# Optimization experiments

Measured on AMD Instinct MI355X. Metric: run time of the kernel, lower is better.

## Reference

```python
import jax, jax.numpy as jnp
import numpy as np

N = 4_194_304      # number of rays
NUM_ITER = 12      # Newton iterations (fixed)
DAMPING = 0.95
TOL = 1e-6
EPS = 1e-12


def setup_inputs() -> dict:
    key = jax.random.key(0)
    k1, k2 = jax.random.split(key, 2)
    # Rays start on the plane x=-10 inside the aperture, pointing roughly +x.
    yz = jax.random.uniform(k1, (N, 2), minval=-20.0, maxval=20.0)
    P = jnp.concatenate([jnp.full((N, 1), -10.0, jnp.float32), yz], axis=1)
    d = jax.random.normal(k2, (N, 2), dtype=jnp.float32) * 0.05
    V = jnp.concatenate([jnp.ones((N, 1), jnp.float32), d], axis=1)
    V = V / jnp.linalg.norm(V, axis=1, keepdims=True)
    return {
        "P": P,
        "V": V,
        "tf": jnp.eye(4, dtype=jnp.float32),
        "diameter": jnp.float32(50.0),
        "C": jnp.float32(0.02),          # curvature 1/R, R = 50mm
        "anchors": jnp.zeros((2,), jnp.float32),
        "scale": jnp.float32(1.0),
        "normalize": jnp.array(False),
    }


def _translate_x(d):
    return jnp.eye(4, dtype=jnp.float32).at[0, 3].set(d)


def reference(P, V, tf, diameter, C, anchors, scale, normalize):
    dtype = P.dtype

    # spherical sag g(r) = C r^2 / (1 + sqrt(1 - C^2 r^2)); dg/dy = C y / sqrt(1 - C^2 r^2)
    def sag(y, z):
        r2 = y * y + z * z
        s = jnp.sqrt(jnp.maximum(1.0 - C * C * r2, EPS))
        g = C * r2 / (1.0 + s)
        return g, C / s  # (sag value, radial derivative factor)

    # Anchor extents (sag at anchor radii) -> surface / next transforms
    half = diameter / 2
    e0, _ = sag(anchors[0] * half, jnp.zeros((), dtype))
    e1, _ = sag(anchors[1] * half, jnp.zeros((), dtype))
    S = jnp.diag(jnp.concatenate([jnp.full((3,), scale, dtype), jnp.ones((1,), dtype)]))
    tf_surface = tf @ _translate_x(-scale * e0) @ S
    tf_next = tf @ _translate_x(scale * (e1 - e0))

    # Rays into surface-local frame
    A = tf_surface[:3, :3]
    b = tf_surface[:3, 3]
    Ainv = jnp.linalg.inv(A)
    Pl = (P - b) @ Ainv.T   # [N,3]
    Vl = V @ Ainv.T         # [N,3]

    tau = jnp.where(normalize, half, jnp.ones((), dtype))

    # Implicit F(p) = (sag(y,z) - x)/tau, gradient (-1, dg/dy, dg/dz)/tau
    def implicit(p):
        x, y, z = p[:, 0], p[:, 1], p[:, 2]
        g, dgd = sag(y, z)
        f = (g - x) / tau
        grad = jnp.stack([-jnp.ones_like(x), dgd * y, dgd * z], axis=-1) / tau
        return f, grad

    # Damped Newton on t along the ray (fixed unroll = num_iter)
    t = jnp.zeros(P.shape[0], dtype)
    for _ in range(NUM_ITER):
        p = Pl + t[:, None] * Vl
        f, grad = implicit(p)
        denom = jnp.sum(grad * Vl, axis=-1)
        denom = jnp.where(jnp.abs(denom) < EPS,
                          jnp.where(denom >= 0, EPS, -EPS), denom)
        t = t - DAMPING * f / denom

    p = Pl + t[:, None] * Vl
    _, grad = implicit(p)

    # Domain check: hit point within lens diameter (with tolerance slack)
    r = jnp.sqrt(p[:, 1] ** 2 + p[:, 2] ** 2)
    valid = r <= half + TOL

    # Normals back to world frame: n_w = Ainv^T @ grad, normalized
    n_w = grad @ Ainv
    normals = n_w / jnp.linalg.norm(n_w, axis=-1, keepdims=True)

    return t, normals, valid, tf_surface, tf_next
```

## Files before the change

### kernel.cpp

```cpp
#include <hip/hip_runtime.h>

#define NUM_ITER 12
#define DAMPING 0.95f
#define TOL 1e-6f
#define EPSF 1e-12f

__device__ __forceinline__ float frcp(float x)  { return __builtin_amdgcn_rcpf(x); }
__device__ __forceinline__ float frsq(float x)  { return __builtin_amdgcn_rsqf(x); }
__device__ __forceinline__ float fsqrt(float x) { return __builtin_amdgcn_sqrtf(x); }

__global__ __launch_bounds__(256) void sphere_trace_kernel(
    const float* __restrict__ P,
    const float* __restrict__ V,
    const float* __restrict__ tf,
    const float* __restrict__ diameter_p,
    const float* __restrict__ C_p,
    const float* __restrict__ anchors,
    const float* __restrict__ scale_p,
    const unsigned char* __restrict__ normalize_p,
    float* __restrict__ out,
    int n)
{
    const float diameter = diameter_p[0];
    const float C        = C_p[0];
    const float scale    = scale_p[0];
    const float half = 0.5f * diameter;

    float a0 = anchors[0] * half;
    float a1 = anchors[1] * half;
    float r2a0 = a0 * a0;
    float r2a1 = a1 * a1;
    float s0 = fsqrt(fmaxf(1.0f - C * C * r2a0, EPSF));
    float s1 = fsqrt(fmaxf(1.0f - C * C * r2a1, EPSF));
    float e0 = C * r2a0 * frcp(1.0f + s0);
    float e1 = C * r2a1 * frcp(1.0f + s1);

    float A[3][3], b[3];
    #pragma unroll
    for (int i = 0; i < 3; ++i) {
        #pragma unroll
        for (int j = 0; j < 3; ++j) A[i][j] = tf[i * 4 + j] * scale;
        b[i] = tf[i * 4 + 3] - scale * e0 * tf[i * 4 + 0];
    }

    float ia = A[0][0], ib = A[0][1], ic = A[0][2];
    float id = A[1][0], ie = A[1][1], ifv = A[1][2];
    float ig = A[2][0], ih = A[2][1], ii = A[2][2];
    float det = ia * (ie * ii - ifv * ih) - ib * (id * ii - ifv * ig) + ic * (id * ih - ie * ig);
    float idet = frcp(det);
    float Ai[3][3];
    Ai[0][0] = (ie * ii - ifv * ih) * idet;
    Ai[0][1] = (ic * ih - ib * ii) * idet;
    Ai[0][2] = (ib * ifv - ic * ie) * idet;
    Ai[1][0] = (ifv * ig - id * ii) * idet;
    Ai[1][1] = (ia * ii - ic * ig) * idet;
    Ai[1][2] = (ic * id - ia * ifv) * idet;
    Ai[2][0] = (id * ih - ie * ig) * idet;
    Ai[2][1] = (ib * ig - ia * ih) * idet;
    Ai[2][2] = (ia * ie - ib * id) * idet;

    const float CC   = C * C;
    const float invC = frcp(C);
    const float rlim = half + TOL;

    const int gid0   = blockIdx.x * blockDim.x + threadIdx.x;
    const int stride = gridDim.x * blockDim.x;

    if (gid0 < 32) {
        int k = gid0;
        int m = k & 15;
        int i = m >> 2, j = m & 3;
        float v;
        if (k < 16) {
            v = (j < 3) ? tf[i * 4 + j] * scale
                        : tf[i * 4 + 3] - scale * e0 * tf[i * 4 + 0];
            out[5 * n + m] = v;
        } else {
            v = (j < 3) ? tf[i * 4 + j]
                        : tf[i * 4 + 3] + scale * (e1 - e0) * tf[i * 4 + 0];
            out[5 * n + 16 + m] = v;
        }
    }

    const int ngroups = n >> 2;

    const float4* __restrict__ P4 = (const float4*)P;
    const float4* __restrict__ V4 = (const float4*)V;

    for (int grp = gid0; grp < ngroups; grp += stride) {
        float4 pa = P4[3 * grp + 0];
        float4 pb = P4[3 * grp + 1];
        float4 pc = P4[3 * grp + 2];
        float4 va = V4[3 * grp + 0];
        float4 vb = V4[3 * grp + 1];
        float4 vc = V4[3 * grp + 2];

        float Px[4] = {pa.x, pa.w, pb.z, pc.y};
        float Py[4] = {pa.y, pb.x, pb.w, pc.z};
        float Pz[4] = {pa.z, pb.y, pc.x, pc.w};
        float Vx[4] = {va.x, va.w, vb.z, vc.y};
        float Vy[4] = {va.y, vb.x, vb.w, vc.z};
        float Vz[4] = {va.z, vb.y, vc.x, vc.w};

        float plx[4], ply[4], plz[4], vlx[4], vly[4], vlz[4], t[4];
        #pragma unroll
        for (int k = 0; k < 4; ++k) {
            float dx = Px[k] - b[0], dy = Py[k] - b[1], dz = Pz[k] - b[2];
            plx[k] = Ai[0][0] * dx + Ai[0][1] * dy + Ai[0][2] * dz;
            ply[k] = Ai[1][0] * dx + Ai[1][1] * dy + Ai[1][2] * dz;
            plz[k] = Ai[2][0] * dx + Ai[2][1] * dy + Ai[2][2] * dz;
            vlx[k] = Ai[0][0] * Vx[k] + Ai[0][1] * Vy[k] + Ai[0][2] * Vz[k];
            vly[k] = Ai[1][0] * Vx[k] + Ai[1][1] * Vy[k] + Ai[1][2] * Vz[k];
            vlz[k] = Ai[2][0] * Vx[k] + Ai[2][1] * Vy[k] + Ai[2][2] * Vz[k];
            t[k] = 0.0f;
        }

        for (int it = 0; it < NUM_ITER; ++it) {
            #pragma unroll
            for (int k = 0; k < 4; ++k) {
                float px = fmaf(t[k], vlx[k], plx[k]);
                float py = fmaf(t[k], vly[k], ply[k]);
                float pz = fmaf(t[k], vlz[k], plz[k]);
                float r2 = fmaf(py, py, pz * pz);
                float s  = fsqrt(fmaxf(fmaf(-CC, r2, 1.0f), EPSF));
                float g  = fmaf(-s, invC, invC);
                float dot = fmaf(py, vly[k], pz * vlz[k]);
                float num = s * (g - px);
                float den = fmaf(-s, vlx[k], C * dot);
                t[k] = fmaf(-DAMPING * num, frcp(den), t[k]);
            }
        }

        float nx[4], ny[4], nz[4], vd[4];
        #pragma unroll
        for (int k = 0; k < 4; ++k) {
            float py = fmaf(t[k], vly[k], ply[k]);
            float pz = fmaf(t[k], vlz[k], plz[k]);
            float r2 = fmaf(py, py, pz * pz);
            float s  = fsqrt(fmaxf(fmaf(-CC, r2, 1.0f), EPSF));
            float dgd = C * frcp(s);
            float gy = dgd * py;
            float gz = dgd * pz;
            float nwx = -Ai[0][0] + gy * Ai[1][0] + gz * Ai[2][0];
            float nwy = -Ai[0][1] + gy * Ai[1][1] + gz * Ai[2][1];
            float nwz = -Ai[0][2] + gy * Ai[1][2] + gz * Ai[2][2];
            float invn = frsq(fmaf(nwx, nwx, fmaf(nwy, nwy, nwz * nwz)));
            nx[k] = nwx * invn; ny[k] = nwy * invn; nz[k] = nwz * invn;
            vd[k] = (fsqrt(r2) <= rlim) ? 1.0f : 0.0f;
        }

        float4* t4 = (float4*)(out) + grp;
        *t4 = make_float4(t[0], t[1], t[2], t[3]);
        float4* n4 = (float4*)(out + n) + 3 * grp;
        n4[0] = make_float4(nx[0], ny[0], nz[0], nx[1]);
        n4[1] = make_float4(ny[1], nz[1], nx[2], ny[2]);
        n4[2] = make_float4(nz[2], nx[3], ny[3], nz[3]);
        float4* v4o = (float4*)(out + 4 * n) + grp;
        *v4o = make_float4(vd[0], vd[1], vd[2], vd[3]);
    }

    const int rem0 = ngroups << 2;
    for (int idx = rem0 + gid0; idx < n; idx += stride) {
        float dx = P[3 * idx + 0] - b[0], dy = P[3 * idx + 1] - b[1], dz = P[3 * idx + 2] - b[2];
        float Vx = V[3 * idx + 0], Vy = V[3 * idx + 1], Vz = V[3 * idx + 2];
        float plx = Ai[0][0] * dx + Ai[0][1] * dy + Ai[0][2] * dz;
        float ply = Ai[1][0] * dx + Ai[1][1] * dy + Ai[1][2] * dz;
        float plz = Ai[2][0] * dx + Ai[2][1] * dy + Ai[2][2] * dz;
        float vlx = Ai[0][0] * Vx + Ai[0][1] * Vy + Ai[0][2] * Vz;
        float vly = Ai[1][0] * Vx + Ai[1][1] * Vy + Ai[1][2] * Vz;
        float vlz = Ai[2][0] * Vx + Ai[2][1] * Vy + Ai[2][2] * Vz;
        float t = 0.0f;
        for (int it = 0; it < NUM_ITER; ++it) {
            float px = fmaf(t, vlx, plx);
            float py = fmaf(t, vly, ply);
            float pz = fmaf(t, vlz, plz);
            float r2 = fmaf(py, py, pz * pz);
            float s  = fsqrt(fmaxf(fmaf(-CC, r2, 1.0f), EPSF));
            float g  = fmaf(-s, invC, invC);
            float dot = fmaf(py, vly, pz * vlz);
            t = fmaf(-DAMPING * (s * (g - px)), frcp(fmaf(-s, vlx, C * dot)), t);
        }
        float py = fmaf(t, vly, ply);
        float pz = fmaf(t, vlz, plz);
        float r2 = fmaf(py, py, pz * pz);
        float s  = fsqrt(fmaxf(fmaf(-CC, r2, 1.0f), EPSF));
        float dgd = C * frcp(s);
        float gy = dgd * py, gz = dgd * pz;
        float nwx = -Ai[0][0] + gy * Ai[1][0] + gz * Ai[2][0];
        float nwy = -Ai[0][1] + gy * Ai[1][1] + gz * Ai[2][1];
        float nwz = -Ai[0][2] + gy * Ai[1][2] + gz * Ai[2][2];
        float invn = frsq(fmaf(nwx, nwx, fmaf(nwy, nwy, nwz * nwz)));
        out[idx] = t;
        out[n + 3 * idx + 0] = nwx * invn;
        out[n + 3 * idx + 1] = nwy * invn;
        out[n + 3 * idx + 2] = nwz * invn;
        out[4 * n + idx] = (fsqrt(r2) <= rlim) ? 1.0f : 0.0f;
    }
}

extern "C" void kernel_launch(void* const* d_in, const int* in_sizes, int n_in,
                              void* d_out, int out_size, void* d_ws, size_t ws_size,
                              hipStream_t stream) {
    const float* P  = (const float*)d_in[0];
    const float* V  = (const float*)d_in[1];
    const float* tf = (const float*)d_in[2];
    const float* diameter = (const float*)d_in[3];
    const float* C        = (const float*)d_in[4];
    const float* anchors  = (const float*)d_in[5];
    const float* scale    = (const float*)d_in[6];
    const unsigned char* normalize = (const unsigned char*)d_in[7];
    float* out = (float*)d_out;

    const int n = in_sizes[0] / 3;

    const int block = 256;
    int blocks = ((n >> 2) + block - 1) / block;
    if (blocks > 4096) blocks = 4096;
    if (blocks < 1) blocks = 1;

    sphere_trace_kernel<<<blocks, block, 0, stream>>>(
        P, V, tf, diameter, C, anchors, scale, normalize, out, n);
}
```

Baseline: 40.99 us.

## Replace damped Newton iterations with closed-form ray-sphere intersection

Replaces the 12-step damped Newton solve for the spherical sag with an analytic ray–sphere quadratic solve, using the stable q-form of the root. The normal is taken directly as the vector from the sphere centre to the hit point, then transformed to world frame and normalized. This removes the per-iteration sqrt, reciprocal and FMA chains, leaving mostly load/store traffic. It relies on the surface being exactly spherical and on the damped iteration having converged. Results may differ slightly where the Newton iteration had not fully converged or where the discriminant is clamped.

New measurement: 34.36 us. 16.2% less time.

```diff
diff --git a/kernel.cpp b/kernel.cpp
--- a/kernel.cpp
+++ b/kernel.cpp
@@ -1,13 +1,12 @@
 #include <hip/hip_runtime.h>
 
-#define NUM_ITER 12
-#define DAMPING 0.95f
 #define TOL 1e-6f
 #define EPSF 1e-12f
 
 __device__ __forceinline__ float frcp(float x)  { return __builtin_amdgcn_rcpf(x); }
 __device__ __forceinline__ float frsq(float x)  { return __builtin_amdgcn_rsqf(x); }
 __device__ __forceinline__ float fsqrt(float x) { return __builtin_amdgcn_sqrtf(x); }
+
 
 __global__ __launch_bounds__(256) void sphere_trace_kernel(
     const float* __restrict__ P,
@@ -59,8 +58,8 @@
     Ai[2][1] = (ib * ig - ia * ih) * idet;
     Ai[2][2] = (ia * ie - ib * id) * idet;
 
-    const float CC   = C * C;
-    const float invC = frcp(C);
+    const float R    = 1.0f / C;
+    const float RR   = R * R;
     const float rlim = half + TOL;
 
     const int gid0   = blockIdx.x * blockDim.x + threadIdx.x;
@@ -102,51 +101,38 @@
         float Vy[4] = {va.y, vb.x, vb.w, vc.z};
         float Vz[4] = {va.z, vb.y, vc.x, vc.w};
 
-        float plx[4], ply[4], plz[4], vlx[4], vly[4], vlz[4], t[4];
+        float t[4], nx[4], ny[4], nz[4], vd[4];
         #pragma unroll
         for (int k = 0; k < 4; ++k) {
             float dx = Px[k] - b[0], dy = Py[k] - b[1], dz = Pz[k] - b[2];
-            plx[k] = Ai[0][0] * dx + Ai[0][1] * dy + Ai[0][2] * dz;
-            ply[k] = Ai[1][0] * dx + Ai[1][1] * dy + Ai[1][2] * dz;
-            plz[k] = Ai[2][0] * dx + Ai[2][1] * dy + Ai[2][2] * dz;
-            vlx[k] = Ai[0][0] * Vx[k] + Ai[0][1] * Vy[k] + Ai[0][2] * Vz[k];
-            vly[k] = Ai[1][0] * Vx[k] + Ai[1][1] * Vy[k] + Ai[1][2] * Vz[k];
-            vlz[k] = Ai[2][0] * Vx[k] + Ai[2][1] * Vy[k] + Ai[2][2] * Vz[k];
-            t[k] = 0.0f;
-        }
-
-        for (int it = 0; it < NUM_ITER; ++it) {
-            #pragma unroll
-            for (int k = 0; k < 4; ++k) {
-                float px = fmaf(t[k], vlx[k], plx[k]);
-                float py = fmaf(t[k], vly[k], ply[k]);
-                float pz = fmaf(t[k], vlz[k], plz[k]);
-                float r2 = fmaf(py, py, pz * pz);
-                float s  = fsqrt(fmaxf(fmaf(-CC, r2, 1.0f), EPSF));
-                float g  = fmaf(-s, invC, invC);
-                float dot = fmaf(py, vly[k], pz * vlz[k]);
-                float num = s * (g - px);
-                float den = fmaf(-s, vlx[k], C * dot);
-                t[k] = fmaf(-DAMPING * num, frcp(den), t[k]);
-            }
-        }
-
-        float nx[4], ny[4], nz[4], vd[4];
-        #pragma unroll
-        for (int k = 0; k < 4; ++k) {
-            float py = fmaf(t[k], vly[k], ply[k]);
-            float pz = fmaf(t[k], vlz[k], plz[k]);
-            float r2 = fmaf(py, py, pz * pz);
-            float s  = fsqrt(fmaxf(fmaf(-CC, r2, 1.0f), EPSF));
-            float dgd = C * frcp(s);
-            float gy = dgd * py;
-            float gz = dgd * pz;
-            float nwx = -Ai[0][0] + gy * Ai[1][0] + gz * Ai[2][0];
-            float nwy = -Ai[0][1] + gy * Ai[1][1] + gz * Ai[2][1];
-            float nwz = -Ai[0][2] + gy * Ai[1][2] + gz * Ai[2][2];
+            float plx = Ai[0][0] * dx + Ai[0][1] * dy + Ai[0][2] * dz;
+            float ply = Ai[1][0] * dx + Ai[1][1] * dy + Ai[1][2] * dz;
+            float plz = Ai[2][0] * dx + Ai[2][1] * dy + Ai[2][2] * dz;
+            float vlx = Ai[0][0] * Vx[k] + Ai[0][1] * Vy[k] + Ai[0][2] * Vz[k];
+            float vly = Ai[1][0] * Vx[k] + Ai[1][1] * Vy[k] + Ai[1][2] * Vz[k];
+            float vlz = Ai[2][0] * Vx[k] + Ai[2][1] * Vy[k] + Ai[2][2] * Vz[k];
+
+            float mx = plx - R;
+            float bb = mx * vlx + ply * vly + plz * vlz;
+            float aa = vlx * vlx + vly * vly + vlz * vlz;
+            float c0 = mx * mx + ply * ply + plz * plz - RR;
+            float D  = fmaxf(bb * bb - aa * c0, 0.0f);
+            float q  = fsqrt(D) - bb;
+            float tt = c0 * frcp(q);
+            t[k] = tt;
+
+            float py = __fadd_rn(ply, __fmul_rn(tt, vly));
+            float pz = __fadd_rn(plz, __fmul_rn(tt, vlz));
+            float r2 = __fadd_rn(__fmul_rn(py, py), __fmul_rn(pz, pz));
+            float r  = sqrtf(r2);
+            vd[k] = (r <= rlim) ? 1.0f : 0.0f;
+
+            float nlx = fmaf(tt, vlx, mx);
+            float nwx = nlx * Ai[0][0] + py * Ai[1][0] + pz * Ai[2][0];
+            float nwy = nlx * Ai[0][1] + py * Ai[1][1] + pz * Ai[2][1];
+            float nwz = nlx * Ai[0][2] + py * Ai[1][2] + pz * Ai[2][2];
             float invn = frsq(fmaf(nwx, nwx, fmaf(nwy, nwy, nwz * nwz)));
             nx[k] = nwx * invn; ny[k] = nwy * invn; nz[k] = nwz * invn;
-            vd[k] = (fsqrt(r2) <= rlim) ? 1.0f : 0.0f;
         }
 
         float4* t4 = (float4*)(out) + grp;
@@ -169,32 +155,26 @@
         float vlx = Ai[0][0] * Vx + Ai[0][1] * Vy + Ai[0][2] * Vz;
         float vly = Ai[1][0] * Vx + Ai[1][1] * Vy + Ai[1][2] * Vz;
         float vlz = Ai[2][0] * Vx + Ai[2][1] * Vy + Ai[2][2] * Vz;
-        float t = 0.0f;
-        for (int it = 0; it < NUM_ITER; ++it) {
-            float px = fmaf(t, vlx, plx);
-            float py = fmaf(t, vly, ply);
-            float pz = fmaf(t, vlz, plz);
-            float r2 = fmaf(py, py, pz * pz);
-            float s  = fsqrt(fmaxf(fmaf(-CC, r2, 1.0f), EPSF));
-            float g  = fmaf(-s, invC, invC);
-            float dot = fmaf(py, vly, pz * vlz);
-            t = fmaf(-DAMPING * (s * (g - px)), frcp(fmaf(-s, vlx, C * dot)), t);
-        }
-        float py = fmaf(t, vly, ply);
-        float pz = fmaf(t, vlz, plz);
-        float r2 = fmaf(py, py, pz * pz);
-        float s  = fsqrt(fmaxf(fmaf(-CC, r2, 1.0f), EPSF));
-        float dgd = C * frcp(s);
-        float gy = dgd * py, gz = dgd * pz;
-        float nwx = -Ai[0][0] + gy * Ai[1][0] + gz * Ai[2][0];
-        float nwy = -Ai[0][1] + gy * Ai[1][1] + gz * Ai[2][1];
-        float nwz = -Ai[0][2] + gy * Ai[1][2] + gz * Ai[2][2];
+        float mx = plx - R;
+        float bb = mx * vlx + ply * vly + plz * vlz;
+        float aa = vlx * vlx + vly * vly + vlz * vlz;
+        float c0 = mx * mx + ply * ply + plz * plz - RR;
+        float D  = fmaxf(bb * bb - aa * c0, 0.0f);
+        float q  = fsqrt(D) - bb;
+        float tt = c0 * frcp(q);
+        float py = __fadd_rn(ply, __fmul_rn(tt, vly));
+        float pz = __fadd_rn(plz, __fmul_rn(tt, vlz));
+        float r2 = __fadd_rn(__fmul_rn(py, py), __fmul_rn(pz, pz));
+        float nlx = fmaf(tt, vlx, mx);
+        float nwx = nlx * Ai[0][0] + py * Ai[1][0] + pz * Ai[2][0];
+        float nwy = nlx * Ai[0][1] + py * Ai[1][1] + pz * Ai[2][1];
+        float nwz = nlx * Ai[0][2] + py * Ai[1][2] + pz * Ai[2][2];
         float invn = frsq(fmaf(nwx, nwx, fmaf(nwy, nwy, nwz * nwz)));
-        out[idx] = t;
+        out[idx] = tt;
         out[n + 3 * idx + 0] = nwx * invn;
         out[n + 3 * idx + 1] = nwy * invn;
         out[n + 3 * idx + 2] = nwz * invn;
-        out[4 * n + idx] = (fsqrt(r2) <= rlim) ? 1.0f : 0.0f;
+        out[4 * n + idx] = (sqrtf(r2) <= rlim) ? 1.0f : 0.0f;
     }
 }
 
```
